# Optimization experiments

Hardware: AMD Instinct MI355X
Metric: run time of the kernel (lower is better)

## Reference

```python
import jax, jax.numpy as jnp
import numpy as np
from jax import lax

B, H, W = 4096, 15, 15
P, V = 16, 32
D = P + V            # 48
PCODE = 2380
NEMB = 2 * (PCODE + 1)  # 4762


def _conv(x, w, b=None, groups=1, pad='SAME'):
    # x: [B,C,H,W], w: [O, I/groups, kh, kw] (torch OIHW layout)
    y = lax.conv_general_dilated(
        x, w, window_strides=(1, 1), padding=pad,
        dimension_numbers=('NCHW', 'OIHW', 'NCHW'),
        feature_group_count=groups)
    if b is not None:
        y = y + b[None, :, None, None]
    return y


def setup_inputs() -> dict:
    key = jax.random.key(0)
    ks = jax.random.split(key, 18)
    f = lambda k, shape: (jax.random.normal(k, shape, jnp.float32) * 0.05)
    inp = {
        'emb': f(ks[0], (NEMB, D)),
        'conv_w': f(ks[1], (D, 1, 3, 3)),      # depthwise, groups=D
        'conv_b': f(ks[2], (D,)),
        'ppw_w': f(ks[3], (P, P, 1, 1)),
        'ppw_b': f(ks[4], (P,)),
        'pdw_w': f(ks[5], (P, 1, 3, 3)),       # depthwise, groups=P
        'pdw_b': f(ks[6], (P,)),
        'pf_w': f(ks[7], (1, P, 1, 1)),        # final policy conv, no bias
        'vpw_w': f(ks[8], (V, V, 1, 1)),
        'vpw_b': f(ks[9], (V,)),
        'vl1_w': f(ks[10], (V, V)),
        'vl1_b': f(ks[11], (V,)),
        'vl2_w': f(ks[12], (V, V)),
        'vl2_b': f(ks[13], (V,)),
        'vf_w': f(ks[14], (3, V)),
        'vf_b': f(ks[15], (3,)),
        'sparse_feature_input': jax.random.randint(ks[16], (B, 12, H, W), 0, PCODE, jnp.int32),
        'board_input': jax.random.randint(ks[17], (B, 2, H, W), 0, 2, jnp.int32),
    }
    return inp


def reference(emb, conv_w, conv_b, ppw_w, ppw_b, pdw_w, pdw_b, pf_w,
              vpw_w, vpw_b, vl1_w, vl1_b, vl2_w, vl2_b, vf_w, vf_b,
              sparse_feature_input, board_input):
    relu = jax.nn.relu
    # --- PatternCodeEmbedding ---
    pcode = sparse_feature_input[:, 10:12]                     # [B,2,H,W]
    pcode = jnp.where(board_input > 0, PCODE, pcode)
    pcode = pcode + jnp.array([0, PCODE + 1], jnp.int32)[None, :, None, None]
    feat = emb[pcode].sum(axis=1)                              # [B,H,W,D]
    feat = jnp.transpose(feat, (0, 3, 1, 2))                   # [B,D,H,W]
    # --- trunk depthwise conv ---
    feat = relu(_conv(feat, conv_w, conv_b, groups=D))
    # --- policy head ---
    pol = feat[:, :P]
    pol = relu(_conv(pol, ppw_w, ppw_b))
    pol = relu(_conv(pol, pdw_w, pdw_b, groups=P))
    pol = _conv(pol, pf_w)                                     # [B,1,H,W]
    # --- value head ---
    val = feat[:, P:]
    val = relu(_conv(val, vpw_w, vpw_b))
    val = jnp.mean(val, axis=(2, 3))                           # [B,V]
    val = relu(val @ vl1_w.T + vl1_b)
    val = relu(val @ vl2_w.T + vl2_b)
    val = val @ vf_w.T + vf_b                                  # [B,3]
    return val, pol
```

## Files before the change

### kernel.cpp

```cpp
#include <hip/hip_runtime.h>
#include <hip/hip_fp16.h>

typedef _Float16 half8  __attribute__((ext_vector_type(8)));
typedef _Float16 half4_t __attribute__((ext_vector_type(4)));
typedef _Float16 half2_t __attribute__((ext_vector_type(2)));
typedef float f32x4 __attribute__((ext_vector_type(4)));

namespace {
constexpr int NT = 256;
constexpr int NPIX = 225;
constexpr int PCODE_C = 2380;

constexpr int AROW = 272;
constexpr int ACG  = 4080;

constexpr int OFF_A     = 0;
constexpr int OFF_POLA0 = 0;
constexpr int OFF_POLA1 = 4080;
constexpr int OFF_XC0   = 8160;
constexpr int OFF_XC1   = 11760;
constexpr int OFF_XC2   = 16320;
constexpr int OFF_XC3   = 19920;
constexpr int OFF_SV    = 23520;
constexpr int OFF_H1    = 23648;
constexpr int OFF_H2    = 23776;
constexpr int OFF_XC4   = 24480;
constexpr int OFF_XC5   = 28080;
constexpr int OFF_ZROW  = 31680;
constexpr int OFF_SLOTA = 31952;
constexpr int OFF_SLOTB = 32272;
constexpr int SMEM_BYTES = 32592;
}

__device__ __forceinline__ half2_t pkrtz(float a, float b) {
    return __builtin_bit_cast(half2_t, __builtin_amdgcn_cvt_pkrtz(a, b));
}
__device__ __forceinline__ void wave_fence() {
    asm volatile("s_waitcnt lgkmcnt(0)" ::: "memory");
}

__global__ __launch_bounds__(NT, 5) void patnet_kernel(
    const float* __restrict__ emb,
    const float* __restrict__ conv_w, const float* __restrict__ conv_b,
    const float* __restrict__ ppw_w,  const float* __restrict__ ppw_b,
    const float* __restrict__ pdw_w,  const float* __restrict__ pdw_b,
    const float* __restrict__ pf_w,
    const float* __restrict__ vpw_w,  const float* __restrict__ vpw_b,
    const float* __restrict__ vl1_w,  const float* __restrict__ vl1_b,
    const float* __restrict__ vl2_w,  const float* __restrict__ vl2_b,
    const float* __restrict__ vf_w,   const float* __restrict__ vf_b,
    const int* __restrict__ sparse,   const int* __restrict__ board,
    float* __restrict__ out, int batch)
{
    __shared__ __align__(16) unsigned char smem[SMEM_BYTES];
    const int tid  = threadIdx.x;
    const int b    = blockIdx.x;
    const int lane = tid & 63;
    const int wave = tid >> 6;

    int c0 = 0, c1 = 0;
    if (tid < NPIX) {
        int s10 = sparse[b * 2700 + 10 * NPIX + tid];
        int s11 = sparse[b * 2700 + 11 * NPIX + tid];
        int b0  = board[b * 450 + tid];
        int b1  = board[b * 450 + NPIX + tid];
        c0 = (b0 > 0) ? PCODE_C : s10;
        c1 = ((b1 > 0) ? PCODE_C : s11) + (PCODE_C + 1);
    }

    auto stage_w = [&](int slotOff, const float* wsrc, const float* bsrc, int cgbase) {
        int i = tid - 96;
        if (i >= 0 && i < 160) {
            int cgl = i / 80, r = i - cgl * 80;
            _Float16 v;
            if (r < 72) {
                int t = r >> 3, j = r & 7;
                v = (_Float16)wsrc[((cgbase + cgl) * 8 + j) * 9 + t];
            } else {
                v = (_Float16)bsrc[(cgbase + cgl) * 8 + (r - 72)];
            }
            ((_Float16*)(smem + slotOff))[i] = v;
        }
    };

    stage_w(OFF_SLOTA, conv_w, conv_b, 4);
    if (tid < 96) {
        for (int i = tid; i < 197; i += 96) {
            unsigned char* dst;
            if (i < 180) {
                int cg = i / 30, r = i - cg * 30;
                int row = r >> 1, colB = (r & 1) * 256;
                dst = smem + OFF_A + cg * ACG + row * AROW + colB;
            } else {
                dst = smem + OFF_ZROW + (i - 180) * 16;
            }
            *(half8*)dst = (half8)(_Float16)0.f;
        }
    }

    if (tid < NPIX) {
        const float* e0 = emb + c0 * 48;
        const float* e1 = emb + c1 * 48;
        int y = tid / 15, x = tid - y * 15;
        unsigned char* abase = smem + OFF_A + y * AROW + (x + 1) * 16;
        #pragma unroll
        for (int g = 0; g < 6; g++) {
            f32x4 x0 = *(const f32x4*)(e0 + g * 8);
            f32x4 x1 = *(const f32x4*)(e0 + g * 8 + 4);
            f32x4 y0 = *(const f32x4*)(e1 + g * 8);
            f32x4 y1 = *(const f32x4*)(e1 + g * 8 + 4);
            f32x4 s0 = x0 + y0, s1 = x1 + y1;
            half2_t q0 = pkrtz(s0.x, s0.y), q1 = pkrtz(s0.z, s0.w);
            half2_t q2 = pkrtz(s1.x, s1.y), q3 = pkrtz(s1.z, s1.w);
            half8 hv = {q0[0], q0[1], q1[0], q1[1], q2[0], q2[1], q3[0], q3[1]};
            *(half8*)(abase + g * ACG) = hv;
        }
    }
    __syncthreads();

    auto do_strip = [&](int t, int cgbase, int slotOff, int xBase) {
        int cgl = t / 45, rem = t - cgl * 45;
        int y = rem / 3, s = rem - y * 3;
        const unsigned char* wb = smem + slotOff + cgl * 160;
        half8 wv[9];
        #pragma unroll
        for (int i = 0; i < 9; i++) wv[i] = *(const half8*)(wb + i * 16);
        half8 bias = *(const half8*)(wb + 144);
        half8 acc[5] = {bias, bias, bias, bias, bias};
        const unsigned char* abase = smem + OFF_A + (cgbase + cgl) * ACG;
        const unsigned char* r0 = (y >= 1)  ? abase + (y - 1) * AROW : smem + OFF_ZROW;
        const unsigned char* r1 = abase + y * AROW;
        const unsigned char* r2 = (y <= 13) ? abase + (y + 1) * AROW : smem + OFF_ZROW;
        int xo = s * 80;
        #pragma unroll
        for (int c = 0; c < 7; c++) {
            half8 v0 = *(const half8*)(r0 + xo + c * 16);
            half8 v1 = *(const half8*)(r1 + xo + c * 16);
            half8 v2 = *(const half8*)(r2 + xo + c * 16);
            #pragma unroll
            for (int o = 0; o < 5; o++) {
                int kx = c - o;
                if (kx >= 0 && kx <= 2) {
                    acc[o] = __builtin_elementwise_fma(v0, wv[kx],     acc[o]);
                    acc[o] = __builtin_elementwise_fma(v1, wv[3 + kx], acc[o]);
                    acc[o] = __builtin_elementwise_fma(v2, wv[6 + kx], acc[o]);
                }
            }
        }
        unsigned char* xw = smem + xBase + cgl * 3600 + (y * 15 + s * 5) * 16;
        #pragma unroll
        for (int o = 0; o < 5; o++)
            *(half8*)(xw + o * 16) = __builtin_elementwise_max(acc[o], (half8)(_Float16)0.f);
    };

    if (tid < 90) do_strip(tid, 4, OFF_SLOTA, OFF_XC4);
    stage_w(OFF_SLOTB, conv_w, conv_b, 2);
    __syncthreads();
    if (tid < 90) do_strip(tid, 2, OFF_SLOTB, OFF_XC2);
    stage_w(OFF_SLOTA, conv_w, conv_b, 0);
    __syncthreads();
    if (tid < 90) do_strip(tid, 0, OFF_SLOTA, OFF_XC0);
    stage_w(OFF_SLOTB, pdw_w, pdw_b, 0);

    const int n = lane & 15, q = lane >> 4;
    const int cgp = lane & 1;
    half8 af_p;
    {
        const float* wp = ppw_w + n * 16 + (q & 1) * 8;
        f32x4 w0 = *(const f32x4*)wp, w1 = *(const f32x4*)(wp + 4);
        half8 t = {(_Float16)w0.x, (_Float16)w0.y, (_Float16)w0.z, (_Float16)w0.w,
                   (_Float16)w1.x, (_Float16)w1.y, (_Float16)w1.z, (_Float16)w1.w};
        af_p = (q < 2) ? t : (half8)(_Float16)0.f;
    }
    f32x4 pb = *(const f32x4*)(ppw_b + q * 4);
    half2_t pf0 = pkrtz(pf_w[cgp * 8 + 0], pf_w[cgp * 8 + 1]);
    half2_t pf1 = pkrtz(pf_w[cgp * 8 + 2], pf_w[cgp * 8 + 3]);
    half2_t pf2 = pkrtz(pf_w[cgp * 8 + 4], pf_w[cgp * 8 + 5]);
    half2_t pf3 = pkrtz(pf_w[cgp * 8 + 6], pf_w[cgp * 8 + 7]);
    half8 af0, af1;
    {
        const float* wp = vpw_w + n * 32 + q * 8;
        f32x4 w0 = *(const f32x4*)wp, w1 = *(const f32x4*)(wp + 4);
        af0 = half8{(_Float16)w0.x, (_Float16)w0.y, (_Float16)w0.z, (_Float16)w0.w,
                    (_Float16)w1.x, (_Float16)w1.y, (_Float16)w1.z, (_Float16)w1.w};
        const float* wp2 = vpw_w + (16 + n) * 32 + q * 8;
        f32x4 v0 = *(const f32x4*)wp2, v1 = *(const f32x4*)(wp2 + 4);
        af1 = half8{(_Float16)v0.x, (_Float16)v0.y, (_Float16)v0.z, (_Float16)v0.w,
                    (_Float16)v1.x, (_Float16)v1.y, (_Float16)v1.z, (_Float16)v1.w};
    }
    f32x4 vb0 = *(const f32x4*)(vpw_b + q * 4);
    f32x4 vb1 = *(const f32x4*)(vpw_b + 16 + q * 4);
    __syncthreads();

    if (wave < 3) {
        if (lane < 60) {
            int cg = lane / 30, r = lane - cg * 30;
            int row = r >> 1, colB = (r & 1) * 256;
            *(half8*)(smem + OFF_POLA0 + cg * ACG + row * AROW + colB) = (half8)(_Float16)0.f;
        }
        half8 wvp[9];
        #pragma unroll
        for (int t = 0; t < 9; t++) wvp[t] = *(const half8*)(smem + OFF_SLOTB + cgp * 160 + t * 16);
        half8 biasp = *(const half8*)(smem + OFF_SLOTB + cgp * 160 + 144);

        const int tlo = (wave == 0) ? 0 : ((wave == 1) ? 3 : 8);
        const int thi = (wave == 0) ? 6 : ((wave == 1) ? 11 : 15);
        const int cg3 = q >> 1;
        const int xbp = (q & 1) ? OFF_XC1 : OFF_XC0;
        for (int t = tlo; t < thi; t++) {
            int p = t * 16 + n;
            int pc = (p > 224) ? 224 : p;
            half8 bf = *(const half8*)(smem + xbp + pc * 16);
            f32x4 d = __builtin_amdgcn_mfma_f32_16x16x32_f16(af_p, bf, (f32x4)(0.f), 0, 0, 0);
            if (p < NPIX) {
                int y = p / 15, x = p - y * 15;
                half2_t lo = pkrtz(fmaxf(d.x + pb.x, 0.f), fmaxf(d.y + pb.y, 0.f));
                half2_t hi = pkrtz(fmaxf(d.z + pb.z, 0.f), fmaxf(d.w + pb.w, 0.f));
                half4_t hv = {lo[0], lo[1], hi[0], hi[1]};
                *(half4_t*)(smem + OFF_POLA0 + cg3 * ACG + y * AROW + (x + 1) * 16 + (q & 1) * 8) = hv;
            }
        }
        wave_fence();

        const int px0 = wave * 75;
        for (int i = 0; i < 3; i++) {
            int idx = i * 64 + lane;
            if (idx < 150) {
                int px = px0 + (idx >> 1);
                int y = px / 15, x = px - y * 15;
                const unsigned char* base = smem + OFF_POLA0 + cgp * ACG;
                const unsigned char* pm = (y > 0)  ? base + (y - 1) * AROW : smem + OFF_ZROW;
                const unsigned char* pz = base + y * AROW;
                const unsigned char* pp = (y < 14) ? base + (y + 1) * AROW : smem + OFF_ZROW;
                int xo = x * 16;
                half8 acc = biasp;
                acc = __builtin_elementwise_fma(*(const half8*)(pm + xo),      wvp[0], acc);
                acc = __builtin_elementwise_fma(*(const half8*)(pm + xo + 16), wvp[1], acc);
                acc = __builtin_elementwise_fma(*(const half8*)(pm + xo + 32), wvp[2], acc);
                acc = __builtin_elementwise_fma(*(const half8*)(pz + xo),      wvp[3], acc);
                acc = __builtin_elementwise_fma(*(const half8*)(pz + xo + 16), wvp[4], acc);
                acc = __builtin_elementwise_fma(*(const half8*)(pz + xo + 32), wvp[5], acc);
                acc = __builtin_elementwise_fma(*(const half8*)(pp + xo),      wvp[6], acc);
                acc = __builtin_elementwise_fma(*(const half8*)(pp + xo + 16), wvp[7], acc);
                acc = __builtin_elementwise_fma(*(const half8*)(pp + xo + 32), wvp[8], acc);
                acc = __builtin_elementwise_max(acc, (half8)(_Float16)0.f);
                float part = 0.f;
                part = __builtin_amdgcn_fdot2(half2_t{acc[0], acc[1]}, pf0, part, false);
                part = __builtin_amdgcn_fdot2(half2_t{acc[2], acc[3]}, pf1, part, false);
                part = __builtin_amdgcn_fdot2(half2_t{acc[4], acc[5]}, pf2, part, false);
                part = __builtin_amdgcn_fdot2(half2_t{acc[6], acc[7]}, pf3, part, false);
                float tot = part + __shfl_xor(part, 1, 64);
                if (cgp == 0) out[3 * batch + b * NPIX + px] = tot;
            }
        }
    } else {
        const int xb = (q < 2) ? (OFF_XC2 + q * 3600) : (OFF_XC4 + (q - 2) * 3600);
        f32x4 a0 = {0.f, 0.f, 0.f, 0.f}, a1 = {0.f, 0.f, 0.f, 0.f};
        for (int t = 0; t < 15; t++) {
            int p = t * 16 + n;
            int pc = (p > 224) ? 224 : p;
            half8 bf = *(const half8*)(smem + xb + pc * 16);
            f32x4 d0 = __builtin_amdgcn_mfma_f32_16x16x32_f16(af0, bf, (f32x4)(0.f), 0, 0, 0);
            f32x4 d1 = __builtin_amdgcn_mfma_f32_16x16x32_f16(af1, bf, (f32x4)(0.f), 0, 0, 0);
            if (p < NPIX) {
                #pragma unroll
                for (int r = 0; r < 4; r++) {
                    a0[r] += fmaxf(d0[r] + vb0[r], 0.f);
                    a1[r] += fmaxf(d1[r] + vb1[r], 0.f);
                }
            }
        }
        #pragma unroll
        for (int s = 1; s < 16; s <<= 1) {
            #pragma unroll
            for (int r = 0; r < 4; r++) {
                a0[r] += __shfl_xor(a0[r], s, 64);
                a1[r] += __shfl_xor(a1[r], s, 64);
            }
        }
        if (n == 0) {
            *(f32x4*)(smem + OFF_SV + q * 16)      = a0 * (1.f / 225.f);
            *(f32x4*)(smem + OFF_SV + 64 + q * 16) = a1 * (1.f / 225.f);
        }
        const int o = lane & 31;
        f32x4 wA[8];
        float b1v = vl1_b[o], b2v = vl2_b[o], b3v = 0.f;
        #pragma unroll
        for (int g = 0; g < 8; g++) wA[g] = *(const f32x4*)(vl1_w + o * 32 + g * 4);
        wave_fence();

        f32x4 wB[8];
        #pragma unroll
        for (int g = 0; g < 8; g++) wB[g] = *(const f32x4*)(vl2_w + o * 32 + g * 4);
        float acc1 = b1v;
        #pragma unroll
        for (int g = 0; g < 8; g++) {
            f32x4 sv = *(const f32x4*)(smem + OFF_SV + g * 16);
            acc1 += sv.x * wA[g].x + sv.y * wA[g].y + sv.z * wA[g].z + sv.w * wA[g].w;
        }
        acc1 = fmaxf(acc1, 0.f);
        if (lane < 32) *(float*)(smem + OFF_H1 + o * 4) = acc1;
        wave_fence();

        f32x4 wC[8];
        if (lane < 3) {
            b3v = vf_b[lane];
            #pragma unroll
            for (int g = 0; g < 8; g++) wC[g] = *(const f32x4*)(vf_w + lane * 32 + g * 4);
        }
        float acc2 = b2v;
        #pragma unroll
        for (int g = 0; g < 8; g++) {
            f32x4 hv = *(const f32x4*)(smem + OFF_H1 + g * 16);
            acc2 += hv.x * wB[g].x + hv.y * wB[g].y + hv.z * wB[g].z + hv.w * wB[g].w;
        }
        acc2 = fmaxf(acc2, 0.f);
        if (lane < 32) *(float*)(smem + OFF_H2 + o * 4) = acc2;
        wave_fence();

        if (lane < 3) {
            float acc3 = b3v;
            #pragma unroll
            for (int g = 0; g < 8; g++) {
                f32x4 hv = *(const f32x4*)(smem + OFF_H2 + g * 16);
                acc3 += hv.x * wC[g].x + hv.y * wC[g].y + hv.z * wC[g].z + hv.w * wC[g].w;
            }
            out[b * 3 + lane] = acc3;
        }
    }
}

extern "C" void kernel_launch(void* const* d_in, const int* in_sizes, int n_in,
                              void* d_out, int out_size, void* d_ws, size_t ws_size,
                              hipStream_t stream) {
    const float* emb    = (const float*)d_in[0];
    const float* conv_w = (const float*)d_in[1];
    const float* conv_b = (const float*)d_in[2];
    const float* ppw_w  = (const float*)d_in[3];
    const float* ppw_b  = (const float*)d_in[4];
    const float* pdw_w  = (const float*)d_in[5];
    const float* pdw_b  = (const float*)d_in[6];
    const float* pf_w   = (const float*)d_in[7];
    const float* vpw_w  = (const float*)d_in[8];
    const float* vpw_b  = (const float*)d_in[9];
    const float* vl1_w  = (const float*)d_in[10];
    const float* vl1_b  = (const float*)d_in[11];
    const float* vl2_w  = (const float*)d_in[12];
    const float* vl2_b  = (const float*)d_in[13];
    const float* vf_w   = (const float*)d_in[14];
    const float* vf_b   = (const float*)d_in[15];
    const int* sparse   = (const int*)d_in[16];
    const int* board    = (const int*)d_in[17];
    float* out = (float*)d_out;

    int batch = in_sizes[16] / 2700;
    patnet_kernel<<<batch, NT, 0, stream>>>(
        emb, conv_w, conv_b, ppw_w, ppw_b, pdw_w, pdw_b, pf_w,
        vpw_w, vpw_b, vl1_w, vl1_b, vl2_w, vl2_b, vf_w, vf_b,
        sparse, board, out, batch);
}
```

Measured before the change: 186.6 us.

## Stage all depthwise weights upfront and run trunk conv in two wide passes

All trunk depthwise conv weights and the policy depthwise weights are now staged into shared memory in one step, replacing per-pass weight slot staging. The trunk conv runs in two passes of 225 threads, each handling 3 channel groups with 3-pixel strips, instead of three passes of 90 threads with 5-pixel strips. Conv outputs are stored interleaved as 48-byte pixel records, and the MFMA reads are adjusted to match. This removes one barrier and uses more of the block's threads, at the cost of more shared memory and launch bounds lowered from 5 to 4 blocks per CU.

```diff
diff --git a/kernel.cpp b/kernel.cpp
--- a/kernel.cpp
+++ b/kernel.cpp
@@ -16,20 +16,15 @@
 
 constexpr int OFF_A     = 0;
 constexpr int OFF_POLA0 = 0;
-constexpr int OFF_POLA1 = 4080;
-constexpr int OFF_XC0   = 8160;
-constexpr int OFF_XC1   = 11760;
-constexpr int OFF_XC2   = 16320;
-constexpr int OFF_XC3   = 19920;
-constexpr int OFF_SV    = 23520;
-constexpr int OFF_H1    = 23648;
-constexpr int OFF_H2    = 23776;
-constexpr int OFF_XC4   = 24480;
-constexpr int OFF_XC5   = 28080;
-constexpr int OFF_ZROW  = 31680;
-constexpr int OFF_SLOTA = 31952;
-constexpr int OFF_SLOTB = 32272;
-constexpr int SMEM_BYTES = 32592;
+constexpr int OFF_XLO   = 12240;
+constexpr int OFF_SV    = 23040;
+constexpr int OFF_H1    = 23168;
+constexpr int OFF_H2    = 23296;
+constexpr int OFF_XHI   = 24480;
+constexpr int OFF_ZROW  = 35280;
+constexpr int OFF_WS    = 35392;
+constexpr int OFF_SLOTP = 36352;
+constexpr int SMEM_BYTES = 36672;
 }
 
 __device__ __forceinline__ half2_t pkrtz(float a, float b) {
@@ -39,7 +34,7 @@
     asm volatile("s_waitcnt lgkmcnt(0)" ::: "memory");
 }
 
-__global__ __launch_bounds__(NT, 5) void patnet_kernel(
+__global__ __launch_bounds__(NT, 4) void patnet_kernel(
     const float* __restrict__ emb,
     const float* __restrict__ conv_w, const float* __restrict__ conv_b,
     const float* __restrict__ ppw_w,  const float* __restrict__ ppw_b,
@@ -68,31 +63,31 @@
         c1 = ((b1 > 0) ? PCODE_C : s11) + (PCODE_C + 1);
     }
 
-    auto stage_w = [&](int slotOff, const float* wsrc, const float* bsrc, int cgbase) {
-        int i = tid - 96;
-        if (i >= 0 && i < 160) {
-            int cgl = i / 80, r = i - cgl * 80;
+    {
+        _Float16* WS = (_Float16*)(smem + OFF_WS);
+        for (int i = tid; i < 480; i += NT) {
+            int cg = i / 80, r = i - cg * 80;
             _Float16 v;
-            if (r < 72) {
-                int t = r >> 3, j = r & 7;
-                v = (_Float16)wsrc[((cgbase + cgl) * 8 + j) * 9 + t];
-            } else {
-                v = (_Float16)bsrc[(cgbase + cgl) * 8 + (r - 72)];
-            }
-            ((_Float16*)(smem + slotOff))[i] = v;
-        }
-    };
-
-    stage_w(OFF_SLOTA, conv_w, conv_b, 4);
-    if (tid < 96) {
-        for (int i = tid; i < 197; i += 96) {
+            if (r < 72) { int t = r >> 3, j = r & 7; v = (_Float16)conv_w[(cg * 8 + j) * 9 + t]; }
+            else        { v = (_Float16)conv_b[cg * 8 + (r - 72)]; }
+            WS[i] = v;
+        }
+        _Float16* WP = (_Float16*)(smem + OFF_SLOTP);
+        if (tid < 160) {
+            int cg = tid / 80, r = tid - cg * 80;
+            _Float16 v;
+            if (r < 72) { int t = r >> 3, j = r & 7; v = (_Float16)pdw_w[(cg * 8 + j) * 9 + t]; }
+            else        { v = (_Float16)pdw_b[cg * 8 + (r - 72)]; }
+            WP[tid] = v;
+        }
+        if (tid < 187) {
             unsigned char* dst;
-            if (i < 180) {
-                int cg = i / 30, r = i - cg * 30;
+            if (tid < 180) {
+                int cg = tid / 30, r = tid - cg * 30;
                 int row = r >> 1, colB = (r & 1) * 256;
                 dst = smem + OFF_A + cg * ACG + row * AROW + colB;
             } else {
-                dst = smem + OFF_ZROW + (i - 180) * 16;
+                dst = smem + OFF_ZROW + (tid - 180) * 16;
             }
             *(half8*)dst = (half8)(_Float16)0.f;
         }
@@ -118,27 +113,28 @@
     }
     __syncthreads();
 
-    auto do_strip = [&](int t, int cgbase, int slotOff, int xBase) {
-        int cgl = t / 45, rem = t - cgl * 45;
-        int y = rem / 3, s = rem - y * 3;
-        const unsigned char* wb = smem + slotOff + cgl * 160;
+    auto do_strip = [&](int t, int cgbase, int xBase) {
+        int cgl = t / 75, rem = t - cgl * 75;
+        int y = rem / 5, s = rem - y * 5;
+        int cg = cgbase + cgl;
+        const unsigned char* wb = smem + OFF_WS + cg * 160;
         half8 wv[9];
         #pragma unroll
         for (int i = 0; i < 9; i++) wv[i] = *(const half8*)(wb + i * 16);
         half8 bias = *(const half8*)(wb + 144);
-        half8 acc[5] = {bias, bias, bias, bias, bias};
-        const unsigned char* abase = smem + OFF_A + (cgbase + cgl) * ACG;
-        const unsigned char* r0 = (y >= 1)  ? abase + (y - 1) * AROW : smem + OFF_ZROW;
-        const unsigned char* r1 = abase + y * AROW;
-        const unsigned char* r2 = (y <= 13) ? abase + (y + 1) * AROW : smem + OFF_ZROW;
-        int xo = s * 80;
-        #pragma unroll
-        for (int c = 0; c < 7; c++) {
-            half8 v0 = *(const half8*)(r0 + xo + c * 16);
-            half8 v1 = *(const half8*)(r1 + xo + c * 16);
-            half8 v2 = *(const half8*)(r2 + xo + c * 16);
+        const unsigned char* abase = smem + OFF_A + cg * ACG;
+        int xo = s * 48;
+        const unsigned char* r0 = (y >= 1)  ? abase + (y - 1) * AROW + xo : smem + OFF_ZROW;
+        const unsigned char* r1 = abase + y * AROW + xo;
+        const unsigned char* r2 = (y <= 13) ? abase + (y + 1) * AROW + xo : smem + OFF_ZROW;
+        half8 acc[3] = {bias, bias, bias};
+        #pragma unroll
+        for (int c = 0; c < 5; c++) {
+            half8 v0 = *(const half8*)(r0 + c * 16);
+            half8 v1 = *(const half8*)(r1 + c * 16);
+            half8 v2 = *(const half8*)(r2 + c * 16);
             #pragma unroll
-            for (int o = 0; o < 5; o++) {
+            for (int o = 0; o < 3; o++) {
                 int kx = c - o;
                 if (kx >= 0 && kx <= 2) {
                     acc[o] = __builtin_elementwise_fma(v0, wv[kx],     acc[o]);
@@ -147,20 +143,15 @@
                 }
             }
         }
-        unsigned char* xw = smem + xBase + cgl * 3600 + (y * 15 + s * 5) * 16;
-        #pragma unroll
-        for (int o = 0; o < 5; o++)
-            *(half8*)(xw + o * 16) = __builtin_elementwise_max(acc[o], (half8)(_Float16)0.f);
+        unsigned char* xw = smem + xBase + (y * 15 + s * 3) * 48 + cgl * 16;
+        #pragma unroll
+        for (int o = 0; o < 3; o++)
+            *(half8*)(xw + o * 48) = __builtin_elementwise_max(acc[o], (half8)(_Float16)0.f);
     };
 
-    if (tid < 90) do_strip(tid, 4, OFF_SLOTA, OFF_XC4);
-    stage_w(OFF_SLOTB, conv_w, conv_b, 2);
+    if (tid < 225) do_strip(tid, 3, OFF_XHI);
     __syncthreads();
-    if (tid < 90) do_strip(tid, 2, OFF_SLOTB, OFF_XC2);
-    stage_w(OFF_SLOTA, conv_w, conv_b, 0);
-    __syncthreads();
-    if (tid < 90) do_strip(tid, 0, OFF_SLOTA, OFF_XC0);
-    stage_w(OFF_SLOTB, pdw_w, pdw_b, 0);
+    if (tid < 225) do_strip(tid, 0, OFF_XLO);
 
     const int n = lane & 15, q = lane >> 4;
     const int cgp = lane & 1;
@@ -200,17 +191,17 @@
         }
         half8 wvp[9];
         #pragma unroll
-        for (int t = 0; t < 9; t++) wvp[t] = *(const half8*)(smem + OFF_SLOTB + cgp * 160 + t * 16);
-        half8 biasp = *(const half8*)(smem + OFF_SLOTB + cgp * 160 + 144);
+        for (int t = 0; t < 9; t++) wvp[t] = *(const half8*)(smem + OFF_SLOTP + cgp * 160 + t * 16);
+        half8 biasp = *(const half8*)(smem + OFF_SLOTP + cgp * 160 + 144);
 
         const int tlo = (wave == 0) ? 0 : ((wave == 1) ? 3 : 8);
         const int thi = (wave == 0) ? 6 : ((wave == 1) ? 11 : 15);
         const int cg3 = q >> 1;
-        const int xbp = (q & 1) ? OFF_XC1 : OFF_XC0;
+        const int xoff = (q & 1) * 16;
         for (int t = tlo; t < thi; t++) {
             int p = t * 16 + n;
             int pc = (p > 224) ? 224 : p;
-            half8 bf = *(const half8*)(smem + xbp + pc * 16);
+            half8 bf = *(const half8*)(smem + OFF_XLO + pc * 48 + xoff);
             f32x4 d = __builtin_amdgcn_mfma_f32_16x16x32_f16(af_p, bf, (f32x4)(0.f), 0, 0, 0);
             if (p < NPIX) {
                 int y = p / 15, x = p - y * 15;
@@ -229,20 +220,20 @@
                 int px = px0 + (idx >> 1);
                 int y = px / 15, x = px - y * 15;
                 const unsigned char* base = smem + OFF_POLA0 + cgp * ACG;
-                const unsigned char* pm = (y > 0)  ? base + (y - 1) * AROW : smem + OFF_ZROW;
-                const unsigned char* pz = base + y * AROW;
-                const unsigned char* pp = (y < 14) ? base + (y + 1) * AROW : smem + OFF_ZROW;
                 int xo = x * 16;
+                const unsigned char* pm = (y > 0)  ? base + (y - 1) * AROW + xo : smem + OFF_ZROW;
+                const unsigned char* pz = base + y * AROW + xo;
+                const unsigned char* pp = (y < 14) ? base + (y + 1) * AROW + xo : smem + OFF_ZROW;
                 half8 acc = biasp;
-                acc = __builtin_elementwise_fma(*(const half8*)(pm + xo),      wvp[0], acc);
-                acc = __builtin_elementwise_fma(*(const half8*)(pm + xo + 16), wvp[1], acc);
-                acc = __builtin_elementwise_fma(*(const half8*)(pm + xo + 32), wvp[2], acc);
-                acc = __builtin_elementwise_fma(*(const half8*)(pz + xo),      wvp[3], acc);
-                acc = __builtin_elementwise_fma(*(const half8*)(pz + xo + 16), wvp[4], acc);
-                acc = __builtin_elementwise_fma(*(const half8*)(pz + xo + 32), wvp[5], acc);
-                acc = __builtin_elementwise_fma(*(const half8*)(pp + xo),      wvp[6], acc);
-                acc = __builtin_elementwise_fma(*(const half8*)(pp + xo + 16), wvp[7], acc);
-                acc = __builtin_elementwise_fma(*(const half8*)(pp + xo + 32), wvp[8], acc);
+                acc = __builtin_elementwise_fma(*(const half8*)(pm),      wvp[0], acc);
+                acc = __builtin_elementwise_fma(*(const half8*)(pm + 16), wvp[1], acc);
+                acc = __builtin_elementwise_fma(*(const half8*)(pm + 32), wvp[2], acc);
+                acc = __builtin_elementwise_fma(*(const half8*)(pz),      wvp[3], acc);
+                acc = __builtin_elementwise_fma(*(const half8*)(pz + 16), wvp[4], acc);
+                acc = __builtin_elementwise_fma(*(const half8*)(pz + 32), wvp[5], acc);
+                acc = __builtin_elementwise_fma(*(const half8*)(pp),      wvp[6], acc);
+                acc = __builtin_elementwise_fma(*(const half8*)(pp + 16), wvp[7], acc);
+                acc = __builtin_elementwise_fma(*(const half8*)(pp + 32), wvp[8], acc);
                 acc = __builtin_elementwise_max(acc, (half8)(_Float16)0.f);
                 float part = 0.f;
                 part = __builtin_amdgcn_fdot2(half2_t{acc[0], acc[1]}, pf0, part, false);
@@ -254,12 +245,12 @@
             }
         }
     } else {
-        const int xb = (q < 2) ? (OFF_XC2 + q * 3600) : (OFF_XC4 + (q - 2) * 3600);
+        const int xb = (q == 0) ? (OFF_XLO + 32) : (OFF_XHI + (q - 1) * 16);
         f32x4 a0 = {0.f, 0.f, 0.f, 0.f}, a1 = {0.f, 0.f, 0.f, 0.f};
         for (int t = 0; t < 15; t++) {
             int p = t * 16 + n;
             int pc = (p > 224) ? 224 : p;
-            half8 bf = *(const half8*)(smem + xb + pc * 16);
+            half8 bf = *(const half8*)(smem + xb + pc * 48);
             f32x4 d0 = __builtin_amdgcn_mfma_f32_16x16x32_f16(af0, bf, (f32x4)(0.f), 0, 0, 0);
             f32x4 d1 = __builtin_amdgcn_mfma_f32_16x16x32_f16(af1, bf, (f32x4)(0.f), 0, 0, 0);
             if (p < NPIX) {
```

Measured after the change: 165.5 us. -11.3%, faster.
